# Kernel tuning notes

Measured on AMD Instinct MI355X. Metric: run time of the kernel, lower is better.

## Reference

```python
import jax, jax.numpy as jnp
import numpy as np


def setup_inputs() -> dict:
    key = jax.random.key(0)
    ks = jax.random.split(key, 8)
    B, T, D, H = 4, 4096, 1024, 64
    scale = D ** -0.5
    return {
        "x": jax.random.normal(ks[0], (B, T, D), dtype=jnp.float32),
        "mask": jax.random.randint(ks[1], (B, T), 0, 2, dtype=jnp.int32),
        "wq": jax.random.normal(ks[2], (H, D), dtype=jnp.float32) * scale,
        "bq": jax.random.normal(ks[3], (H,), dtype=jnp.float32) * 0.02,
        "wk": jax.random.normal(ks[4], (H, D), dtype=jnp.float32) * scale,
        "bk": jax.random.normal(ks[5], (H,), dtype=jnp.float32) * 0.02,
        "wv": jax.random.normal(ks[6], (H, D), dtype=jnp.float32) * scale,
        "bv": jax.random.normal(ks[7], (H,), dtype=jnp.float32) * 0.02,
    }


def reference(x, mask, wq, bq, wk, bk, wv, bv):
    # x: [B,T,D]; wq/wk/wv: [H,D] (torch Linear convention), mask: [B,T] int
    head_size = wq.shape[0]
    q = jnp.einsum("btd,hd->bth", x, wq) + bq  # [B,T,H]
    k = jnp.einsum("btd,hd->bth", x, wk) + bk
    v = jnp.einsum("btd,hd->bth", x, wv) + bv
    attn = jnp.einsum("bth,bsh->bts", q, k) * (head_size ** -0.5)  # [B,T,T]
    pad_mask = mask.astype(bool)[:, None, :]  # [B,1,T], True = keep
    attn = jnp.where(pad_mask, attn, jnp.float32(-1e9))
    attn = jax.nn.softmax(attn, axis=-1)
    # dropout is identity in eval/deterministic mode
    return jnp.einsum("bts,bsh->bth", attn, v)  # [B,T,H]
```

## Files before the change

### kernel.cpp

```cpp
#include <hip/hip_runtime.h>
#include <math.h>

#define BATCH 4
#define SEQ   4096
#define DIM   1024
#define HEAD  64
#define MROWS (BATCH*SEQ)
#define KT    64
#define QBLK  64

typedef __attribute__((ext_vector_type(8))) short short8;
typedef __attribute__((ext_vector_type(4))) short s16x4;
typedef __attribute__((ext_vector_type(4))) float f32x4;

static __device__ __forceinline__ unsigned short f2b(float f) {
    union { float f; unsigned u; } v; v.f = f;
    return (unsigned short)((v.u + 0x7FFFu + ((v.u >> 16) & 1u)) >> 16);
}

#define QSC (0.125f * 1.4426950408889634f)
__global__ __launch_bounds__(256) void wconv_kernel(
    const float* __restrict__ wq, const float* __restrict__ bq,
    const float* __restrict__ wk, const float* __restrict__ bk,
    const float* __restrict__ wv, const float* __restrict__ bv,
    unsigned short* __restrict__ Wb, float* __restrict__ biasAll)
{
    int idx = blockIdx.x * 256 + threadIdx.x;
    int e   = idx * 4;
    int row = e >> 10;
    int col = e & 1023;
    const float* src = (row < 64) ? wq : (row < 128) ? wk : wv;
    float s = (row < 64) ? QSC : 1.0f;
    float4 g = *(const float4*)&src[(size_t)(row & 63) * DIM + col];
    ushort4 o;
    o.x = f2b(g.x * s); o.y = f2b(g.y * s); o.z = f2b(g.z * s); o.w = f2b(g.w * s);
    *(ushort4*)&Wb[e] = o;
    if (idx < 192) {
        const float* bs = (idx < 64) ? bq : (idx < 128) ? bk : bv;
        biasAll[idx] = bs[idx & 63] * ((idx < 64) ? QSC : 1.0f);
    }
}

#define NIT (DIM / 32)
__global__ __launch_bounds__(256) void qkvmm_kernel(
    const float* __restrict__ x, const unsigned short* __restrict__ Wb,
    const float* __restrict__ biasAll,
    unsigned short* __restrict__ qout, unsigned short* __restrict__ kout,
    unsigned short* __restrict__ vtout)
{
    __shared__ unsigned short xs[2][32 * 32];
    __shared__ unsigned short ws[2][192 * 32];

    const int tid  = threadIdx.x;
    const int m0   = blockIdx.x * 32;
    const int bb   = m0 >> 12;
    const int lane = tid & 63;
    const int w    = tid >> 6;
    const int lr   = lane & 15;
    const int lg   = lane >> 4;
    const int mrow  = (w >> 1) * 16;
    const int nbase = (w & 1) * 6;

    const int sxrow = tid >> 2, sxlg = tid & 3;
    int wn[3], wlg[3];
    #pragma unroll
    for (int i = 0; i < 3; ++i) { int idx = tid + i * 256; wn[i] = idx >> 2; wlg[i] = idx & 3; }

    f32x4 acc[6];
    #pragma unroll
    for (int nt = 0; nt < 6; ++nt) acc[nt] = (f32x4){0.f, 0.f, 0.f, 0.f};

    float4 xg0, xg1;
    short8 wg[3];

    auto LOADR = [&](int ko) {
        if (tid < 128) {
            const float* xp = &x[(size_t)(m0 + sxrow) * DIM + ko + sxlg * 8];
            xg0 = *(const float4*)xp;
            xg1 = *(const float4*)(xp + 4);
        }
        #pragma unroll
        for (int i = 0; i < 3; ++i)
            wg[i] = *(const short8*)&Wb[(size_t)wn[i] * DIM + ko + wlg[i] * 8];
    };
    auto WRITE = [&](int buf) {
        if (tid < 128) {
            short8 c;
            c[0] = (short)f2b(xg0.x); c[1] = (short)f2b(xg0.y);
            c[2] = (short)f2b(xg0.z); c[3] = (short)f2b(xg0.w);
            c[4] = (short)f2b(xg1.x); c[5] = (short)f2b(xg1.y);
            c[6] = (short)f2b(xg1.z); c[7] = (short)f2b(xg1.w);
            *(short8*)&xs[buf][sxrow * 32 + ((sxlg * 8) ^ ((sxrow & 3) * 8))] = c;
        }
        #pragma unroll
        for (int i = 0; i < 3; ++i)
            *(short8*)&ws[buf][wn[i] * 32 + ((wlg[i] * 8) ^ ((wn[i] & 3) * 8))] = wg[i];
    };

    LOADR(0);
    WRITE(0);
    __syncthreads();

    for (int it = 0; it < NIT; ++it) {
        if (it + 1 < NIT) LOADR((it + 1) * 32);
        const int cur = it & 1;
        const int arow = mrow + lr;
        short8 af = *(const short8*)&xs[cur][arow * 32 + ((lg * 8) ^ ((arow & 3) * 8))];
        #pragma unroll
        for (int nt = 0; nt < 6; ++nt) {
            int n = (nbase + nt) * 16 + lr;
            short8 bf = *(const short8*)&ws[cur][n * 32 + ((lg * 8) ^ ((n & 3) * 8))];
            acc[nt] = __builtin_amdgcn_mfma_f32_16x16x32_bf16(af, bf, acc[nt], 0, 0, 0);
        }
        if (it + 1 < NIT) WRITE((it + 1) & 1);
        __syncthreads();
    }

    #pragma unroll
    for (int nt = 0; nt < 6; ++nt) {
        int gn = (nbase + nt) * 16 + lr;
        float bv_ = biasAll[gn];
        #pragma unroll
        for (int r = 0; r < 4; ++r) {
            int grow = m0 + mrow + lg * 4 + r;
            unsigned short val = f2b(acc[nt][r] + bv_);
            if (gn < 64)       qout[(size_t)grow * HEAD + gn] = val;
            else if (gn < 128) kout[(size_t)grow * HEAD + gn - 64] = val;
            else {
                int t = (m0 & 4095) + mrow + lg * 4 + r;
                vtout[((size_t)bb * HEAD + gn - 128) * SEQ + t] = val;
            }
        }
    }
}

__global__ __launch_bounds__(256, 4) void flashmm_kernel(
    const unsigned short* __restrict__ qb, const unsigned short* __restrict__ kb,
    const unsigned short* __restrict__ vt, const int* __restrict__ mask,
    float* __restrict__ opart, float* __restrict__ mpart, float* __restrict__ lpart,
    int nsplit)
{
    const int b  = blockIdx.y;
    const int t0 = blockIdx.x * QBLK;
    const int z  = blockIdx.z;
    const int tid  = threadIdx.x;
    const int lane = tid & 63;
    const int w    = tid >> 6;
    const int lr = lane & 15;
    const int lg = lane >> 4;
    const int span = SEQ / nsplit;
    const int s_begin = z * span, s_end = s_begin + span;

    __shared__ unsigned short ks_l[KT * HEAD];
    __shared__ unsigned short vt_l[HEAD * KT];
    __shared__ unsigned short ps_l[4][16 * KT];
    __shared__ float mkf[KT];
    __shared__ float sf_l[4][16];

    const unsigned short* qrow = qb + ((size_t)(b * SEQ + t0 + w * 16 + lr)) * HEAD;
    const short8 qf0 = *(const short8*)(qrow + lg * 8);
    const short8 qf1 = *(const short8*)(qrow + 32 + lg * 8);

    f32x4 acc_o[4];
    #pragma unroll
    for (int nt = 0; nt < 4; ++nt) acc_o[nt] = (f32x4){0.f, 0.f, 0.f, 0.f};
    float m_r = -INFINITY, l_r = 0.f;

    short8 kg[2], vg[2];
    float mgf = 0.f;

    auto LOADR = [&](int st) {
        #pragma unroll
        for (int i = 0; i < 2; ++i) {
            int c   = tid + i * 256;
            int row = c >> 3;
            int h0  = (c & 7) * 8;
            kg[i] = *(const short8*)(kb + ((size_t)(b * SEQ + st + row)) * HEAD + h0);
            vg[i] = *(const short8*)(vt + ((size_t)(b * HEAD + row)) * SEQ + st + h0);
        }
        if (tid < KT) mgf = (mask[(size_t)b * SEQ + st + tid] != 0) ? 0.f : -1e9f;
    };
    auto WRITE = [&]() {
        #pragma unroll
        for (int i = 0; i < 2; ++i) {
            int c   = tid + i * 256;
            int row = c >> 3;
            int h0  = (c & 7) * 8;
            *(short8*)&ks_l[row * HEAD + (h0 ^ ((row & 7) << 3))] = kg[i];
            *(short8*)&vt_l[row * KT + (h0 ^ ((row & 7) << 3))] = vg[i];
        }
        if (tid < KT) mkf[tid] = mgf;
    };

    LOADR(s_begin);
    for (int st = s_begin; st < s_end; st += KT) {
        __syncthreads();
        WRITE();
        __syncthreads();
        if (st + KT < s_end) LOADR(st + KT);

        f32x4 sT[4];
        __builtin_amdgcn_s_setprio(1);
        #pragma unroll
        for (int ct = 0; ct < 4; ++ct) {
            int krow = ct * 16 + lr;
            short8 kf0 = *(const short8*)&ks_l[krow * HEAD + ((lg * 8) ^ ((krow & 7) << 3))];
            short8 kf1 = *(const short8*)&ks_l[krow * HEAD + ((32 + lg * 8) ^ ((krow & 7) << 3))];
            f32x4 zz = (f32x4){0.f, 0.f, 0.f, 0.f};
            zz = __builtin_amdgcn_mfma_f32_16x16x32_bf16(kf0, qf0, zz, 0, 0, 0);
            zz = __builtin_amdgcn_mfma_f32_16x16x32_bf16(kf1, qf1, zz, 0, 0, 0);
            sT[ct] = zz;
        }
        __builtin_amdgcn_s_setprio(0);

        #pragma unroll
        for (int ct = 0; ct < 4; ++ct) {
            f32x4 mb = *(const f32x4*)&mkf[ct * 16 + lg * 4];
            sT[ct][0] += mb[0]; sT[ct][1] += mb[1];
            sT[ct][2] += mb[2]; sT[ct][3] += mb[3];
        }

        float mx = sT[0][0];
        #pragma unroll
        for (int ct = 0; ct < 4; ++ct)
            #pragma unroll
            for (int r = 0; r < 4; ++r) mx = fmaxf(mx, sT[ct][r]);
        mx = fmaxf(mx, __shfl_xor(mx, 16));
        mx = fmaxf(mx, __shfl_xor(mx, 32));
        float mnew = fmaxf(m_r, mx);

        float rs = 0.f;
        #pragma unroll
        for (int ct = 0; ct < 4; ++ct)
            #pragma unroll
            for (int r = 0; r < 4; ++r) {
                float p = __builtin_amdgcn_exp2f(sT[ct][r] - mnew);
                sT[ct][r] = p;
                rs += p;
            }
        rs += __shfl_xor(rs, 16);
        rs += __shfl_xor(rs, 32);
        float sf = __builtin_amdgcn_exp2f(m_r - mnew);
        l_r = l_r * sf + rs;
        m_r = mnew;
        if (lg == 0) sf_l[w][lr] = sf;

        #pragma unroll
        for (int ct = 0; ct < 4; ++ct) {
            s16x4 pk;
            pk[0] = (short)f2b(sT[ct][0]); pk[1] = (short)f2b(sT[ct][1]);
            pk[2] = (short)f2b(sT[ct][2]); pk[3] = (short)f2b(sT[ct][3]);
            *(s16x4*)&ps_l[w][lr * KT + ((ct * 16 + lg * 4) ^ ((lr & 7) << 3))] = pk;
        }

        f32x4 sfv = *(const f32x4*)&sf_l[w][lg * 4];
        #pragma unroll
        for (int nt = 0; nt < 4; ++nt) {
            acc_o[nt][0] *= sfv[0]; acc_o[nt][1] *= sfv[1];
            acc_o[nt][2] *= sfv[2]; acc_o[nt][3] *= sfv[3];
        }

        __builtin_amdgcn_s_setprio(1);
        #pragma unroll
        for (int kk = 0; kk < 2; ++kk) {
            int s0 = kk * 32 + lg * 8;
            short8 pf = *(const short8*)&ps_l[w][lr * KT + (s0 ^ ((lr & 7) << 3))];
            #pragma unroll
            for (int nt = 0; nt < 4; ++nt) {
                int hrow = nt * 16 + lr;
                short8 vf = *(const short8*)&vt_l[hrow * KT + (s0 ^ ((hrow & 7) << 3))];
                acc_o[nt] = __builtin_amdgcn_mfma_f32_16x16x32_bf16(pf, vf, acc_o[nt], 0, 0, 0);
            }
        }
        __builtin_amdgcn_s_setprio(0);
    }

    const size_t rbase = (size_t)z * MROWS + (size_t)b * SEQ + t0 + w * 16;
    const size_t obase = rbase * HEAD;
    #pragma unroll
    for (int nt = 0; nt < 4; ++nt)
        #pragma unroll
        for (int r = 0; r < 4; ++r) {
            int R = lg * 4 + r;
            opart[obase + (size_t)R * HEAD + nt * 16 + lr] = acc_o[nt][r];
        }
    if (lg == 0) {
        mpart[rbase + lr] = m_r;
        lpart[rbase + lr] = l_r;
    }
}

__global__ __launch_bounds__(256) void combine_kernel(
    const float* __restrict__ op, const float* __restrict__ mp,
    const float* __restrict__ lp, float* __restrict__ out, int nsplit)
{
    int idx = blockIdx.x * 256 + threadIdx.x;
    int row = idx >> 4;
    int h4  = (idx & 15) * 4;
    float mstar = -INFINITY;
    for (int s = 0; s < nsplit; ++s)
        mstar = fmaxf(mstar, mp[(size_t)s * MROWS + row]);
    float L = 0.f;
    float ax = 0.f, ay = 0.f, az = 0.f, aw = 0.f;
    for (int s = 0; s < nsplit; ++s) {
        float wgt = __builtin_amdgcn_exp2f(mp[(size_t)s * MROWS + row] - mstar);
        L += lp[(size_t)s * MROWS + row] * wgt;
        float4 o = *(const float4*)&op[((size_t)s * MROWS + row) * HEAD + h4];
        ax += o.x * wgt; ay += o.y * wgt; az += o.z * wgt; aw += o.w * wgt;
    }
    float r = 1.f / L;
    float4 res; res.x = ax * r; res.y = ay * r; res.z = az * r; res.w = aw * r;
    *(float4*)&out[(size_t)row * HEAD + h4] = res;
}

extern "C" void kernel_launch(void* const* d_in, const int* in_sizes, int n_in,
                              void* d_out, int out_size, void* d_ws, size_t ws_size,
                              hipStream_t stream) {
    const float* x    = (const float*)d_in[0];
    const int*   mask = (const int*)d_in[1];
    const float* wq   = (const float*)d_in[2];
    const float* bq   = (const float*)d_in[3];
    const float* wk   = (const float*)d_in[4];
    const float* bk   = (const float*)d_in[5];
    const float* wv   = (const float*)d_in[6];
    const float* bv   = (const float*)d_in[7];
    float* out = (float*)d_out;
    (void)in_sizes; (void)n_in; (void)out_size;

    const size_t NB = (size_t)MROWS * HEAD;
    unsigned short* qw  = (unsigned short*)d_ws;
    unsigned short* kw  = qw + NB;
    unsigned short* vtw = kw + NB;
    unsigned short* Wb  = vtw + NB;
    float* biasAll = (float*)(Wb + (size_t)192 * DIM);
    float* mpart   = biasAll + 192;

    const size_t base = 3 * NB * 2 + (size_t)192 * DIM * 2 + 192 * 4;
    const size_t per  = (size_t)MROWS * 8 + NB * 4;
    int KS = 1;
    if      (ws_size >= base + 8 * per) KS = 8;
    else if (ws_size >= base + 4 * per) KS = 4;
    else if (ws_size >= base + 2 * per) KS = 2;

    float* lpart = mpart + (size_t)KS * MROWS;
    float* opart = lpart + (size_t)KS * MROWS;

    wconv_kernel<<<dim3(192), 256, 0, stream>>>(wq, bq, wk, bk, wv, bv, Wb, biasAll);
    qkvmm_kernel<<<dim3(MROWS / 32), 256, 0, stream>>>(x, Wb, biasAll, qw, kw, vtw);
    flashmm_kernel<<<dim3(SEQ / QBLK, BATCH, KS), 256, 0, stream>>>(qw, kw, vtw, mask,
                                                                    opart, mpart, lpart, KS);
    combine_kernel<<<dim3(MROWS * 16 / 256), 256, 0, stream>>>(opart, mpart, lpart, out, KS);
}
```

Before: 78.58 us.

## Process two query tiles per attention block with lazy rescaling and packed bf16 converts

Each attention block now covers 128 query rows, with every wave handling two 16-row query tiles. Each K/V tile staged in shared memory is therefore reused by twice as many rows, halving K/V global and LDS loads per query. It also skips the running-max rescale of the accumulator when the new max stays within 8 (log2 units) of the old one, drops the sf_l shared-memory round trip in favour of lane shuffles, and replaces the hand-written bf16 rounding with the v_cvt_pk_bf16_f32 instruction. The cost is more registers per thread and half as many blocks in the grid, which may lower occupancy.

```diff
diff --git a/kernel.cpp b/kernel.cpp
--- a/kernel.cpp
+++ b/kernel.cpp
@@ -7,15 +7,19 @@
 #define HEAD  64
 #define MROWS (BATCH*SEQ)
 #define KT    64
-#define QBLK  64
+#define QBLK  128
 
 typedef __attribute__((ext_vector_type(8))) short short8;
-typedef __attribute__((ext_vector_type(4))) short s16x4;
 typedef __attribute__((ext_vector_type(4))) float f32x4;
 
 static __device__ __forceinline__ unsigned short f2b(float f) {
     union { float f; unsigned u; } v; v.f = f;
     return (unsigned short)((v.u + 0x7FFFu + ((v.u >> 16) & 1u)) >> 16);
+}
+static __device__ __forceinline__ unsigned cvtpk(float a, float b) {
+    unsigned r;
+    asm("v_cvt_pk_bf16_f32 %0, %1, %2" : "=v"(r) : "v"(a), "v"(b));
+    return r;
 }
 
 #define QSC (0.125f * 1.4426950408889634f)
@@ -85,12 +89,10 @@
     };
     auto WRITE = [&](int buf) {
         if (tid < 128) {
-            short8 c;
-            c[0] = (short)f2b(xg0.x); c[1] = (short)f2b(xg0.y);
-            c[2] = (short)f2b(xg0.z); c[3] = (short)f2b(xg0.w);
-            c[4] = (short)f2b(xg1.x); c[5] = (short)f2b(xg1.y);
-            c[6] = (short)f2b(xg1.z); c[7] = (short)f2b(xg1.w);
-            *(short8*)&xs[buf][sxrow * 32 + ((sxlg * 8) ^ ((sxrow & 3) * 8))] = c;
+            uint4 c;
+            c.x = cvtpk(xg0.x, xg0.y); c.y = cvtpk(xg0.z, xg0.w);
+            c.z = cvtpk(xg1.x, xg1.y); c.w = cvtpk(xg1.z, xg1.w);
+            *(uint4*)&xs[buf][sxrow * 32 + ((sxlg * 8) ^ ((sxrow & 3) * 8))] = c;
         }
         #pragma unroll
         for (int i = 0; i < 3; ++i)
@@ -153,140 +155,169 @@
 
     __shared__ unsigned short ks_l[KT * HEAD];
     __shared__ unsigned short vt_l[HEAD * KT];
-    __shared__ unsigned short ps_l[4][16 * KT];
+    __shared__ unsigned short ps_l[4][2 * 16 * KT];
     __shared__ float mkf[KT];
-    __shared__ float sf_l[4][16];
-
-    const unsigned short* qrow = qb + ((size_t)(b * SEQ + t0 + w * 16 + lr)) * HEAD;
-    const short8 qf0 = *(const short8*)(qrow + lg * 8);
-    const short8 qf1 = *(const short8*)(qrow + 32 + lg * 8);
-
-    f32x4 acc_o[4];
-    #pragma unroll
-    for (int nt = 0; nt < 4; ++nt) acc_o[nt] = (f32x4){0.f, 0.f, 0.f, 0.f};
-    float m_r = -INFINITY, l_r = 0.f;
-
-    short8 kg[2], vg[2];
+
+    short8 qf[2][2];
+    #pragma unroll
+    for (int u = 0; u < 2; ++u) {
+        const unsigned short* qrow = qb + ((size_t)(b * SEQ + t0 + u * 64 + w * 16 + lr)) * HEAD;
+        qf[u][0] = *(const short8*)(qrow + lg * 8);
+        qf[u][1] = *(const short8*)(qrow + 32 + lg * 8);
+    }
+
+    f32x4 acc_o[2][4];
+    #pragma unroll
+    for (int u = 0; u < 2; ++u)
+        #pragma unroll
+        for (int nt = 0; nt < 4; ++nt) acc_o[u][nt] = (f32x4){0.f, 0.f, 0.f, 0.f};
+    float m_r[2] = {-INFINITY, -INFINITY};
+    float l_r[2] = {0.f, 0.f};
+
+    const int srow0 = tid >> 3, sh0 = (tid & 7) * 8;
+    const unsigned short* kp0 = kb + ((size_t)(b * SEQ + s_begin + srow0)) * HEAD + sh0;
+    const unsigned short* kp1 = kp0 + (size_t)32 * HEAD;
+    const unsigned short* vp0 = vt + ((size_t)(b * HEAD + srow0)) * SEQ + s_begin + sh0;
+    const unsigned short* vp1 = vp0 + (size_t)32 * SEQ;
+    const int* mp_ = mask + (size_t)b * SEQ + s_begin + tid;
+
+    const int kw_off0 = srow0 * HEAD + (sh0 ^ ((srow0 & 7) << 3));
+    const int kw_off1 = (srow0 + 32) * HEAD + (sh0 ^ (((srow0 + 32) & 7) << 3));
+    const int vw_off0 = srow0 * KT + (sh0 ^ ((srow0 & 7) << 3));
+    const int vw_off1 = (srow0 + 32) * KT + (sh0 ^ (((srow0 + 32) & 7) << 3));
+
+    short8 kg0, kg1, vg0, vg1;
     float mgf = 0.f;
 
-    auto LOADR = [&](int st) {
-        #pragma unroll
-        for (int i = 0; i < 2; ++i) {
-            int c   = tid + i * 256;
-            int row = c >> 3;
-            int h0  = (c & 7) * 8;
-            kg[i] = *(const short8*)(kb + ((size_t)(b * SEQ + st + row)) * HEAD + h0);
-            vg[i] = *(const short8*)(vt + ((size_t)(b * HEAD + row)) * SEQ + st + h0);
-        }
-        if (tid < KT) mgf = (mask[(size_t)b * SEQ + st + tid] != 0) ? 0.f : -1e9f;
+    auto LOADR = [&]() {
+        kg0 = *(const short8*)kp0; kg1 = *(const short8*)kp1;
+        vg0 = *(const short8*)vp0; vg1 = *(const short8*)vp1;
+        if (tid < KT) mgf = (*mp_ != 0) ? 0.f : -1e9f;
+        kp0 += (size_t)KT * HEAD; kp1 += (size_t)KT * HEAD;
+        vp0 += KT; vp1 += KT; mp_ += KT;
     };
     auto WRITE = [&]() {
-        #pragma unroll
-        for (int i = 0; i < 2; ++i) {
-            int c   = tid + i * 256;
-            int row = c >> 3;
-            int h0  = (c & 7) * 8;
-            *(short8*)&ks_l[row * HEAD + (h0 ^ ((row & 7) << 3))] = kg[i];
-            *(short8*)&vt_l[row * KT + (h0 ^ ((row & 7) << 3))] = vg[i];
-        }
+        *(short8*)&ks_l[kw_off0] = kg0; *(short8*)&ks_l[kw_off1] = kg1;
+        *(short8*)&vt_l[vw_off0] = vg0; *(short8*)&vt_l[vw_off1] = vg1;
         if (tid < KT) mkf[tid] = mgf;
     };
 
-    LOADR(s_begin);
+    unsigned short* psw = &ps_l[w][0];
+
+    LOADR();
     for (int st = s_begin; st < s_end; st += KT) {
         __syncthreads();
         WRITE();
         __syncthreads();
-        if (st + KT < s_end) LOADR(st + KT);
-
-        f32x4 sT[4];
+        if (st + KT < s_end) LOADR();
+
+        f32x4 sT[2][4];
         __builtin_amdgcn_s_setprio(1);
         #pragma unroll
         for (int ct = 0; ct < 4; ++ct) {
             int krow = ct * 16 + lr;
             short8 kf0 = *(const short8*)&ks_l[krow * HEAD + ((lg * 8) ^ ((krow & 7) << 3))];
             short8 kf1 = *(const short8*)&ks_l[krow * HEAD + ((32 + lg * 8) ^ ((krow & 7) << 3))];
-            f32x4 zz = (f32x4){0.f, 0.f, 0.f, 0.f};
-            zz = __builtin_amdgcn_mfma_f32_16x16x32_bf16(kf0, qf0, zz, 0, 0, 0);
-            zz = __builtin_amdgcn_mfma_f32_16x16x32_bf16(kf1, qf1, zz, 0, 0, 0);
-            sT[ct] = zz;
+            #pragma unroll
+            for (int u = 0; u < 2; ++u) {
+                f32x4 zz = (f32x4){0.f, 0.f, 0.f, 0.f};
+                zz = __builtin_amdgcn_mfma_f32_16x16x32_bf16(kf0, qf[u][0], zz, 0, 0, 0);
+                zz = __builtin_amdgcn_mfma_f32_16x16x32_bf16(kf1, qf[u][1], zz, 0, 0, 0);
+                sT[u][ct] = zz;
+            }
         }
         __builtin_amdgcn_s_setprio(0);
 
         #pragma unroll
         for (int ct = 0; ct < 4; ++ct) {
             f32x4 mb = *(const f32x4*)&mkf[ct * 16 + lg * 4];
-            sT[ct][0] += mb[0]; sT[ct][1] += mb[1];
-            sT[ct][2] += mb[2]; sT[ct][3] += mb[3];
-        }
-
-        float mx = sT[0][0];
-        #pragma unroll
-        for (int ct = 0; ct < 4; ++ct)
-            #pragma unroll
-            for (int r = 0; r < 4; ++r) mx = fmaxf(mx, sT[ct][r]);
-        mx = fmaxf(mx, __shfl_xor(mx, 16));
-        mx = fmaxf(mx, __shfl_xor(mx, 32));
-        float mnew = fmaxf(m_r, mx);
-
-        float rs = 0.f;
-        #pragma unroll
-        for (int ct = 0; ct < 4; ++ct)
-            #pragma unroll
-            for (int r = 0; r < 4; ++r) {
-                float p = __builtin_amdgcn_exp2f(sT[ct][r] - mnew);
-                sT[ct][r] = p;
-                rs += p;
-            }
-        rs += __shfl_xor(rs, 16);
-        rs += __shfl_xor(rs, 32);
-        float sf = __builtin_amdgcn_exp2f(m_r - mnew);
-        l_r = l_r * sf + rs;
-        m_r = mnew;
-        if (lg == 0) sf_l[w][lr] = sf;
-
-        #pragma unroll
-        for (int ct = 0; ct < 4; ++ct) {
-            s16x4 pk;
-            pk[0] = (short)f2b(sT[ct][0]); pk[1] = (short)f2b(sT[ct][1]);
-            pk[2] = (short)f2b(sT[ct][2]); pk[3] = (short)f2b(sT[ct][3]);
-            *(s16x4*)&ps_l[w][lr * KT + ((ct * 16 + lg * 4) ^ ((lr & 7) << 3))] = pk;
-        }
-
-        f32x4 sfv = *(const f32x4*)&sf_l[w][lg * 4];
-        #pragma unroll
-        for (int nt = 0; nt < 4; ++nt) {
-            acc_o[nt][0] *= sfv[0]; acc_o[nt][1] *= sfv[1];
-            acc_o[nt][2] *= sfv[2]; acc_o[nt][3] *= sfv[3];
+            #pragma unroll
+            for (int u = 0; u < 2; ++u) {
+                sT[u][ct][0] += mb[0]; sT[u][ct][1] += mb[1];
+                sT[u][ct][2] += mb[2]; sT[u][ct][3] += mb[3];
+            }
+        }
+
+        #pragma unroll
+        for (int u = 0; u < 2; ++u) {
+            float mx = sT[u][0][0];
+            #pragma unroll
+            for (int ct = 0; ct < 4; ++ct)
+                #pragma unroll
+                for (int r = 0; r < 4; ++r) mx = fmaxf(mx, sT[u][ct][r]);
+            mx = fmaxf(mx, __shfl_xor(mx, 16));
+            mx = fmaxf(mx, __shfl_xor(mx, 32));
+
+            bool defer = __all(mx <= m_r[u] + 8.f);
+            float base = defer ? m_r[u] : fmaxf(m_r[u], mx);
+
+            float rs = 0.f;
+            #pragma unroll
+            for (int ct = 0; ct < 4; ++ct)
+                #pragma unroll
+                for (int r = 0; r < 4; ++r) {
+                    float p = __builtin_amdgcn_exp2f(sT[u][ct][r] - base);
+                    sT[u][ct][r] = p;
+                    rs += p;
+                }
+            rs += __shfl_xor(rs, 16);
+            rs += __shfl_xor(rs, 32);
+
+            if (defer) {
+                l_r[u] += rs;
+            } else {
+                float sf = __builtin_amdgcn_exp2f(m_r[u] - base);
+                l_r[u] = l_r[u] * sf + rs;
+                m_r[u] = base;
+                #pragma unroll
+                for (int r = 0; r < 4; ++r) {
+                    float sfr = __shfl(sf, lg * 4 + r);
+                    #pragma unroll
+                    for (int nt = 0; nt < 4; ++nt) acc_o[u][nt][r] *= sfr;
+                }
+            }
+
+            #pragma unroll
+            for (int ct = 0; ct < 4; ++ct) {
+                uint2 pk;
+                pk.x = cvtpk(sT[u][ct][0], sT[u][ct][1]);
+                pk.y = cvtpk(sT[u][ct][2], sT[u][ct][3]);
+                *(uint2*)&psw[u * (16 * KT) + lr * KT + ((ct * 16 + lg * 4) ^ ((lr & 7) << 3))] = pk;
+            }
         }
 
         __builtin_amdgcn_s_setprio(1);
         #pragma unroll
         for (int kk = 0; kk < 2; ++kk) {
             int s0 = kk * 32 + lg * 8;
-            short8 pf = *(const short8*)&ps_l[w][lr * KT + (s0 ^ ((lr & 7) << 3))];
+            short8 pf0 = *(const short8*)&psw[0 * (16 * KT) + lr * KT + (s0 ^ ((lr & 7) << 3))];
+            short8 pf1 = *(const short8*)&psw[1 * (16 * KT) + lr * KT + (s0 ^ ((lr & 7) << 3))];
             #pragma unroll
             for (int nt = 0; nt < 4; ++nt) {
                 int hrow = nt * 16 + lr;
                 short8 vf = *(const short8*)&vt_l[hrow * KT + (s0 ^ ((hrow & 7) << 3))];
-                acc_o[nt] = __builtin_amdgcn_mfma_f32_16x16x32_bf16(pf, vf, acc_o[nt], 0, 0, 0);
+                acc_o[0][nt] = __builtin_amdgcn_mfma_f32_16x16x32_bf16(pf0, vf, acc_o[0][nt], 0, 0, 0);
+                acc_o[1][nt] = __builtin_amdgcn_mfma_f32_16x16x32_bf16(pf1, vf, acc_o[1][nt], 0, 0, 0);
             }
         }
         __builtin_amdgcn_s_setprio(0);
     }
 
-    const size_t rbase = (size_t)z * MROWS + (size_t)b * SEQ + t0 + w * 16;
-    const size_t obase = rbase * HEAD;
-    #pragma unroll
-    for (int nt = 0; nt < 4; ++nt)
-        #pragma unroll
-        for (int r = 0; r < 4; ++r) {
-            int R = lg * 4 + r;
-            opart[obase + (size_t)R * HEAD + nt * 16 + lr] = acc_o[nt][r];
-        }
-    if (lg == 0) {
-        mpart[rbase + lr] = m_r;
-        lpart[rbase + lr] = l_r;
+    #pragma unroll
+    for (int u = 0; u < 2; ++u) {
+        const size_t rbase = (size_t)z * MROWS + (size_t)b * SEQ + t0 + u * 64 + w * 16;
+        const size_t obase = rbase * HEAD;
+        #pragma unroll
+        for (int nt = 0; nt < 4; ++nt)
+            #pragma unroll
+            for (int r = 0; r < 4; ++r) {
+                int R = lg * 4 + r;
+                opart[obase + (size_t)R * HEAD + nt * 16 + lr] = acc_o[u][nt][r];
+            }
+        if (lg == 0) {
+            mpart[rbase + lr] = m_r[u];
+            lpart[rbase + lr] = l_r[u];
+        }
     }
 }
 
```

Result: slower. 145.2 us (+84.8%).
